# Performance work log

Hardware: AMD Instinct MI355X
Metric: run time of the kernel (lower is better)

The kernel has to match this reference:

```python
import jax, jax.numpy as jnp
import numpy as np

N = 20000        # nodes
E = 320000       # edges (avg degree 16)
F_IN = 128       # node_features
F2 = 64          # second_features (per-head out dim, LSTM hidden)
H = 8            # heads
D1 = H * F2      # 512, concat output of GATConv / LSTM input
NEG_SLOPE = 0.2  # GATConv default leaky_relu slope


def _gat_conv(x, src, dst, W, att_src, att_dst, bias):
    """PyG GATConv (concat=True, self-loops added, eval-mode dropout)."""
    n = x.shape[0]
    h = (x @ W).reshape(n, H, -1)                      # [N,H,F]
    a_s = (h * att_src).sum(-1)                        # [N,H]
    a_d = (h * att_dst).sum(-1)                        # [N,H]
    e = jax.nn.leaky_relu(a_s[src] + a_d[dst], NEG_SLOPE)   # [E',H]
    m = jax.ops.segment_max(e, dst, num_segments=n)    # [N,H]
    m = jnp.where(jnp.isfinite(m), m, 0.0)
    ex = jnp.exp(e - m[dst])
    denom = jax.ops.segment_sum(ex, dst, num_segments=n)
    alpha = ex / (denom[dst] + 1e-16)                  # [E',H]
    msg = h[src] * alpha[:, :, None]                   # [E',H,F]
    out = jax.ops.segment_sum(msg, dst, num_segments=n)  # [N,H,F]
    return out.reshape(n, -1) + bias                   # [N,H*F]


def _lstm_step(x, W_ih, W_hh, b_ih, b_hh):
    """Single-timestep PyTorch LSTM with zero initial (h0, c0). x: [N,D1]."""
    h0 = jnp.zeros((x.shape[0], F2), x.dtype)
    gates = x @ W_ih.T + b_ih + h0 @ W_hh.T + b_hh     # [N,4*F2]
    i, f, g, o = jnp.split(gates, 4, axis=-1)
    c = jax.nn.sigmoid(f) * 0.0 + jax.nn.sigmoid(i) * jnp.tanh(g)
    h = jax.nn.sigmoid(o) * jnp.tanh(c)
    return h, (h, c)


def setup_inputs() -> dict:
    key = jax.random.key(0)
    ks = jax.random.split(key, 16)

    def glorot(k, shape, fan_in):
        return jax.random.normal(k, shape, jnp.float32) * (1.0 / np.sqrt(fan_in))

    return {
        "x": jax.random.normal(ks[0], (N, F_IN), jnp.float32),
        "edge_index": jax.random.randint(ks[1], (2, E), 0, N, jnp.int32),
        "edge_weight": jax.random.uniform(ks[2], (E,), jnp.float32),
        # GATConv 1: F_IN -> H*F2
        "W1": glorot(ks[3], (F_IN, H * F2), F_IN),
        "att_src1": glorot(ks[4], (H, F2), F2),
        "att_dst1": glorot(ks[5], (H, F2), F2),
        "bias1": jnp.zeros((H * F2,), jnp.float32),
        # LSTM: input D1 -> hidden F2
        "W_ih": glorot(ks[6], (4 * F2, D1), D1),
        "W_hh": glorot(ks[7], (4 * F2, F2), F2),
        "b_ih": jnp.zeros((4 * F2,), jnp.float32),
        "b_hh": jnp.zeros((4 * F2,), jnp.float32),
        # GATConv 2: F2 -> H*F2
        "W2": glorot(ks[8], (F2, H * F2), F2),
        "att_src2": glorot(ks[9], (H, F2), F2),
        "att_dst2": glorot(ks[10], (H, F2), F2),
        "bias2": jnp.zeros((H * F2,), jnp.float32),
    }


def reference(x, edge_index, edge_weight, W1, att_src1, att_dst1, bias1,
              W_ih, W_hh, b_ih, b_hh, W2, att_src2, att_dst2, bias2):
    # edge_weight is accepted but unused, matching the original forward.
    loops = jnp.arange(N, dtype=edge_index.dtype)
    src = jnp.concatenate([edge_index[0], loops])      # add self-loops (PyG default)
    dst = jnp.concatenate([edge_index[1], loops])

    h = _gat_conv(x, src, dst, W1, att_src1, att_dst1, bias1)   # [N,512]
    h, hidden2 = _lstm_step(h, W_ih, W_hh, b_ih, b_hh)          # [N,64]
    h = jax.nn.relu(h)
    h = _gat_conv(h, src, dst, W2, att_src2, att_dst2, bias2)   # [N,512]
    return jax.nn.softmax(h, axis=1)
```

## Files before the change

kernel.cpp:

```cpp
#include <hip/hip_runtime.h>
#include <math.h>
#include <stdint.h>


__global__ void count_kernel(const int* __restrict__ dst, int* __restrict__ deg, int E) {
  int i = blockIdx.x * 256 + threadIdx.x;
  if (i < E) atomicAdd(&deg[dst[i]], 1);
}

__global__ void scan_kernel(const int* __restrict__ deg, int* __restrict__ rowptr, int n) {
  __shared__ int buf[1024];
  const int tid = threadIdx.x;
  const int i0 = tid * 20;
  int v[20];
  int tsum = 0;
#pragma unroll
  for (int k = 0; k < 20; ++k) {
    int i = i0 + k;
    v[k] = (i < n) ? (deg[i] + 1) : 0;
    tsum += v[k];
  }
  int incl = tsum;
  buf[tid] = incl;
  __syncthreads();
  for (int s = 1; s < 1024; s <<= 1) {
    int t = (tid >= (unsigned)s) ? buf[tid - s] : 0;
    __syncthreads();
    incl += t;
    buf[tid] = incl;
    __syncthreads();
  }
  int excl = incl - tsum;
#pragma unroll
  for (int k = 0; k < 20; ++k) {
    int i = i0 + k;
    if (i < n) rowptr[i] = excl;
    excl += v[k];
  }
  if (tid == 1023) rowptr[n] = incl;
}

__global__ void scatter_kernel(const int* __restrict__ src, const int* __restrict__ dst,
                               const int* __restrict__ rowptr, int* __restrict__ wp,
                               int* __restrict__ col, int E, int n) {
  int i = blockIdx.x * 256 + threadIdx.x;
  if (i < E) {
    int d = dst[i];
    int p = rowptr[d] + atomicAdd(&wp[d], 1);
    col[p] = src[i];
  } else if (i < E + n) {
    int d = i - E;
    int p = rowptr[d] + atomicAdd(&wp[d], 1);
    col[p] = d;
  }
}


__device__ __forceinline__ uint16_t bf16r(float x) {
  uint32_t u = __float_as_uint(x);
  return (uint16_t)((u + 0x7FFFu + ((u >> 16) & 1u)) >> 16);
}
__device__ __forceinline__ void bfsplit(float x, uint16_t& h, uint16_t& l) {
  h = bf16r(x);
  float hf = __uint_as_float((uint32_t)h << 16);
  l = bf16r(x - hf);
}
__device__ __forceinline__ void store4split(uint16_t* oh, uint16_t* ol, float4 v) {
  ushort4 h, l;
  bfsplit(v.x, h.x, l.x); bfsplit(v.y, h.y, l.y);
  bfsplit(v.z, h.z, l.z); bfsplit(v.w, h.w, l.w);
  *reinterpret_cast<ushort4*>(oh) = h;
  *reinterpret_cast<ushort4*>(ol) = l;
}

__device__ __forceinline__ void gload16(const uint16_t* g, uint16_t* l) {
  __builtin_amdgcn_global_load_lds(
      (const __attribute__((address_space(1))) uint32_t*)g,
      (__attribute__((address_space(3))) uint32_t*)l, 16, 0, 0);
}

using bf16x8 = __attribute__((ext_vector_type(8))) short;
using f32x4  = __attribute__((ext_vector_type(4))) float;


template <bool SPLIT_OUT>
__global__ __launch_bounds__(256) void gemm_mfma(
    const uint16_t* __restrict__ Ah, const uint16_t* __restrict__ Al,
    const uint16_t* __restrict__ Bh, const uint16_t* __restrict__ Bl,
    float* __restrict__ C, uint16_t* __restrict__ Ch, uint16_t* __restrict__ Cl,
    const float* __restrict__ bias,
    int M, int K, int lda, int aZ, int bZ, int ldc, int cZ, int biasZ) {
  constexpr int BM = 64, BN = 64, BK = 64;
  constexpr int PL = BM * BK;
  __shared__ __align__(16) uint16_t sAh[2 * PL], sAl[2 * PL];
  __shared__ __align__(16) uint16_t sBh[2 * PL], sBl[2 * PL];
  const int z = blockIdx.z;
  Ah += (size_t)z * aZ; Al += (size_t)z * aZ;
  Bh += (size_t)z * bZ; Bl += (size_t)z * bZ;
  const int tid = threadIdx.x;
  const int wid = tid >> 6, lane = tid & 63;
  int L = blockIdx.x + gridDim.x * blockIdx.y;
  int nwg = gridDim.x * gridDim.y;
  int q = nwg >> 3, r = nwg & 7;
  int xcd = L & 7, gix = L >> 3;
  int base = (xcd < r) ? xcd * (q + 1) : r * (q + 1) + (xcd - r) * q;
  int w = base + gix;
  const int bm = (w / gridDim.x) * BM;
  const int bn = (w % gridDim.x) * BN;
  const int fr = lane & 15;
  const int kg = lane >> 4;
  const int mbase = wid * 16;
  f32x4 acc[4] = {};

  auto stage = [&](int sb, int k0) {
#pragma unroll
    for (int j = 0; j < 2; ++j) {
      int idx = (wid * 2 + j) * 64 + lane;
      int row = idx >> 3, c = idx & 7;
      int rg = min(bm + row, M - 1);
      size_t goA = (size_t)rg * lda + k0 + ((c ^ (row & 7)) << 3);
      uint16_t* ldst = sAh + sb * PL + (wid * 2 + j) * 512;
      gload16(Ah + goA, ldst);
      gload16(Al + goA, sAl + sb * PL + (wid * 2 + j) * 512);
      size_t goB = (size_t)(bn + row) * K + k0 + ((c ^ (row & 7)) << 3);
      gload16(Bh + goB, sBh + sb * PL + (wid * 2 + j) * 512);
      gload16(Bl + goB, sBl + sb * PL + (wid * 2 + j) * 512);
    }
  };

  stage(0, 0);
  __syncthreads();
  int buf = 0;
  for (int k0 = 0; k0 < K; k0 += BK) {
    const bool more = (k0 + BK) < K;
    if (more) stage(buf ^ 1, k0 + BK);
    const char* pAh = (const char*)sAh + buf * (PL * 2);
    const char* pAl = (const char*)sAl + buf * (PL * 2);
    const char* pBh = (const char*)sBh + buf * (PL * 2);
    const char* pBl = (const char*)sBl + buf * (PL * 2);
#pragma unroll
    for (int ks = 0; ks < 2; ++ks) {
      const int kc = ks * 4 + kg;
      bf16x8 ah, al, bh[4], bl[4];
      {
        int m = mbase + fr;
        int off = m * 128 + ((kc ^ (m & 7)) << 4);
        ah = *reinterpret_cast<const bf16x8*>(pAh + off);
        al = *reinterpret_cast<const bf16x8*>(pAl + off);
      }
#pragma unroll
      for (int j = 0; j < 4; ++j) {
        int n = j * 16 + fr;
        int off = n * 128 + ((kc ^ (n & 7)) << 4);
        bh[j] = *reinterpret_cast<const bf16x8*>(pBh + off);
        bl[j] = *reinterpret_cast<const bf16x8*>(pBl + off);
      }
#pragma unroll
      for (int j = 0; j < 4; ++j) {
        acc[j] = __builtin_amdgcn_mfma_f32_16x16x32_bf16(ah, bh[j], acc[j], 0, 0, 0);
        acc[j] = __builtin_amdgcn_mfma_f32_16x16x32_bf16(al, bh[j], acc[j], 0, 0, 0);
        acc[j] = __builtin_amdgcn_mfma_f32_16x16x32_bf16(ah, bl[j], acc[j], 0, 0, 0);
      }
    }
    if (more) {
      __syncthreads();
      buf ^= 1;
    }
  }
  float bz[4];
#pragma unroll
  for (int j = 0; j < 4; ++j)
    bz[j] = bias ? bias[(size_t)z * biasZ + bn + j * 16 + fr] : 0.f;
  if (SPLIT_OUT) {
    Ch += (size_t)z * cZ;
    Cl += (size_t)z * cZ;
  } else {
    C += (size_t)z * cZ;
  }
  {
    int mr = bm + mbase + kg * 4;
#pragma unroll
    for (int rr = 0; rr < 4; ++rr) {
      int m = mr + rr;
      if (m < M) {
#pragma unroll
        for (int j = 0; j < 4; ++j) {
          float v = acc[j][rr] + bz[j];
          size_t o = (size_t)m * ldc + bn + j * 16 + fr;
          if (SPLIT_OUT) {
            uint16_t h, l;
            bfsplit(v, h, l);
            Ch[o] = h; Cl[o] = l;
          } else {
            C[o] = v;
          }
        }
      }
    }
  }
}


__global__ void prep_all_kernel(const float* __restrict__ W_ih, const float* __restrict__ b_ih,
                                const float* __restrict__ b_hh, const float* __restrict__ W1,
                                const float* __restrict__ as1, const float* __restrict__ ad1,
                                const float* __restrict__ W2, const float* __restrict__ as2,
                                const float* __restrict__ ad2,
                                int* __restrict__ degwp,
                                uint16_t* __restrict__ Wtbh, uint16_t* __restrict__ Wtbl,
                                uint16_t* __restrict__ Bt1h, uint16_t* __restrict__ Bt1l,
                                uint16_t* __restrict__ Bt2h, uint16_t* __restrict__ Bt2l,
                                float* __restrict__ bsum, float* __restrict__ watt1,
                                float* __restrict__ watt2, int n2) {
  int idx = blockIdx.x * 256 + threadIdx.x;
  if (idx < n2) {
    degwp[idx] = 0;
    return;
  }
  int t = idx - n2;
  if (t < 98304) {
    int jp = t >> 9, k = t & 511;
    int j = (jp < 64) ? jp : jp + 64;
    uint16_t h, l;
    bfsplit(W_ih[(size_t)j * 512 + k], h, l);
    Wtbh[t] = h; Wtbl[t] = l;
    return;
  }
  t -= 98304;
  if (t < 65536) {
    int n = t >> 7, k = t & 127;
    uint16_t h, l;
    bfsplit(W1[(size_t)k * 512 + n], h, l);
    Bt1h[t] = h; Bt1l[t] = l;
    return;
  }
  t -= 65536;
  if (t < 32768) {
    int n = t >> 6, k = t & 63;
    uint16_t h, l;
    bfsplit(W2[(size_t)k * 512 + n], h, l);
    Bt2h[t] = h; Bt2l[t] = l;
    return;
  }
  t -= 32768;
  if (t < 192) {
    int j = (t < 64) ? t : t + 64;
    bsum[t] = b_ih[j] + b_hh[j];
    return;
  }
  t -= 192;
  if (t < 2048) {
    int f = t >> 4, c = t & 15;
    int k = c & 7;
    const float* att = ((c < 8) ? as1 : ad1) + k * 64;
    const float* w = W1 + (size_t)f * 512 + k * 64;
    float s = 0.f;
#pragma unroll
    for (int j = 0; j < 64; ++j) s = fmaf(w[j], att[j], s);
    watt1[t] = s;
    return;
  }
  t -= 2048;
  if (t < 1024) {
    int f = t >> 4, c = t & 15;
    int k = c & 7;
    const float* att = ((c < 8) ? as2 : ad2) + k * 64;
    const float* w = W2 + (size_t)f * 512 + k * 64;
    float s = 0.f;
#pragma unroll
    for (int j = 0; j < 64; ++j) s = fmaf(w[j], att[j], s);
    watt2[t] = s;
  }
}


template <int F>
__global__ __launch_bounds__(256) void attcoef_kernel(
    const float* __restrict__ feat, const float* __restrict__ watt,
    float* __restrict__ a_s, float* __restrict__ a_d, int n) {
  __shared__ float rows[16 * F];
  __shared__ float wbuf[F * 16];
  const int n0 = blockIdx.x * 16;
  const int tid = threadIdx.x;
  if (n0 + 16 <= n) {
    const float4* g = reinterpret_cast<const float4*>(feat + (size_t)n0 * F);
    float4* l = reinterpret_cast<float4*>(rows);
    for (int i = tid; i < 16 * F / 4; i += 256) l[i] = g[i];
  } else {
    for (int i = tid; i < 16 * F; i += 256) {
      int r = i / F;
      rows[i] = (n0 + r < n) ? feat[(size_t)(n0 + r) * F + (i - r * F)] : 0.f;
    }
  }
  {
    const float4* g = reinterpret_cast<const float4*>(watt);
    float4* l = reinterpret_cast<float4*>(wbuf);
    for (int i = tid; i < F * 16 / 4; i += 256) l[i] = g[i];
  }
  __syncthreads();
  const int local = tid >> 4, c = tid & 15;
  float s = 0.f;
#pragma unroll 8
  for (int f = 0; f < F; ++f) s = fmaf(rows[local * F + f], wbuf[f * 16 + c], s);
  const int node = n0 + local;
  if (node < n) {
    if (c < 8) a_s[(size_t)node * 8 + c] = s;
    else       a_d[(size_t)node * 8 + (c - 8)] = s;
  }
}


template <int F>
__global__ __launch_bounds__(256) void gat_aggregate_wave(
    const float* __restrict__ feat, const float* __restrict__ a_s,
    const float* __restrict__ a_d, const int* __restrict__ rowptr,
    const int* __restrict__ col, uint16_t* __restrict__ aggH,
    uint16_t* __restrict__ aggL, int n) {
  constexpr int F4 = F / 4;
  constexpr int HPG = (F == 128) ? 4 : 2;
  __shared__ float s_alpha[4][8][8];
  __shared__ int s_cols[4][8];
  const int wid = threadIdx.x >> 6;
  const int lane = threadIdx.x & 63;
  const int node = blockIdx.x * 4 + wid;
  if (node >= n) return;
  const int start = rowptr[node];
  const int deg = rowptr[node + 1] - start;
  const int j = lane >> 3;
  const int h = lane & 7;
  const float adh = a_d[(size_t)node * 8 + h];
  float den = 0.f;
  for (int e = j; e < deg; e += 8) {
    int s = col[start + e];
    float v = a_s[(size_t)s * 8 + h] + adh;
    v = (v > 0.f) ? v : 0.2f * v;
    den += __expf(v);
  }
  den += __shfl_xor(den, 8);
  den += __shfl_xor(den, 16);
  den += __shfl_xor(den, 32);
  const float inv = 1.f / (den + 1e-16f);
  const int f4 = lane & (F4 - 1);
  const int hbase = (lane / F4) * HPG;
  float4 acc0 = make_float4(0.f, 0.f, 0.f, 0.f);
  float4 acc1 = make_float4(0.f, 0.f, 0.f, 0.f);
  float4 acc2 = make_float4(0.f, 0.f, 0.f, 0.f);
  float4 acc3 = make_float4(0.f, 0.f, 0.f, 0.f);
  for (int c0 = 0; c0 < deg; c0 += 8) {
    float aval = 0.f;
    int sj = 0;
    if (c0 + j < deg) {
      sj = col[start + c0 + j];
      float v = a_s[(size_t)sj * 8 + h] + adh;
      v = (v > 0.f) ? v : 0.2f * v;
      aval = __expf(v) * inv;
    }
    s_alpha[wid][j][h] = aval;
    if (h == 0) s_cols[wid][j] = sj;
    __builtin_amdgcn_wave_barrier();
    const int ce = min(8, deg - c0);
    for (int e = 0; e < ce; ++e) {
      int s = s_cols[wid][e];
      float4 fv = *reinterpret_cast<const float4*>(feat + (size_t)s * F + f4 * 4);
      if constexpr (HPG == 4) {
        float4 al = *reinterpret_cast<const float4*>(&s_alpha[wid][e][hbase]);
        acc0.x = fmaf(al.x, fv.x, acc0.x); acc0.y = fmaf(al.x, fv.y, acc0.y);
        acc0.z = fmaf(al.x, fv.z, acc0.z); acc0.w = fmaf(al.x, fv.w, acc0.w);
        acc1.x = fmaf(al.y, fv.x, acc1.x); acc1.y = fmaf(al.y, fv.y, acc1.y);
        acc1.z = fmaf(al.y, fv.z, acc1.z); acc1.w = fmaf(al.y, fv.w, acc1.w);
        acc2.x = fmaf(al.z, fv.x, acc2.x); acc2.y = fmaf(al.z, fv.y, acc2.y);
        acc2.z = fmaf(al.z, fv.z, acc2.z); acc2.w = fmaf(al.z, fv.w, acc2.w);
        acc3.x = fmaf(al.w, fv.x, acc3.x); acc3.y = fmaf(al.w, fv.y, acc3.y);
        acc3.z = fmaf(al.w, fv.z, acc3.z); acc3.w = fmaf(al.w, fv.w, acc3.w);
      } else {
        float2 al = *reinterpret_cast<const float2*>(&s_alpha[wid][e][hbase]);
        acc0.x = fmaf(al.x, fv.x, acc0.x); acc0.y = fmaf(al.x, fv.y, acc0.y);
        acc0.z = fmaf(al.x, fv.z, acc0.z); acc0.w = fmaf(al.x, fv.w, acc0.w);
        acc1.x = fmaf(al.y, fv.x, acc1.x); acc1.y = fmaf(al.y, fv.y, acc1.y);
        acc1.z = fmaf(al.y, fv.z, acc1.z); acc1.w = fmaf(al.y, fv.w, acc1.w);
      }
    }
    __builtin_amdgcn_wave_barrier();
  }
  size_t basep = (size_t)node * 8 * F + (size_t)hbase * F + f4 * 4;
  store4split(aggH + basep, aggL + basep, acc0);
  store4split(aggH + basep + F, aggL + basep + F, acc1);
  if constexpr (HPG == 4) {
    store4split(aggH + basep + 2 * F, aggL + basep + 2 * F, acc2);
    store4split(aggH + basep + 3 * F, aggL + basep + 3 * F, acc3);
  }
}


__global__ __launch_bounds__(256) void lstm_act_attcoef_kernel(
    const float* __restrict__ gates, const float* __restrict__ bsum,
    const float* __restrict__ watt2, float* __restrict__ h2,
    float* __restrict__ a_s2, float* __restrict__ a_d2, int n) {
  __shared__ float h2t[4][64];
  __shared__ float wbuf[64 * 16];
  const int tid = threadIdx.x;
  reinterpret_cast<float4*>(wbuf)[tid] = reinterpret_cast<const float4*>(watt2)[tid];
  const int nl = tid >> 6, j = tid & 63;
  const int node = blockIdx.x * 4 + nl;
  float hv = 0.f;
  if (node < n) {
    const float* g0 = gates + (size_t)node * 192;
    float iv = g0[j] + bsum[j];
    float gv = g0[64 + j] + bsum[64 + j];
    float ov = g0[128 + j] + bsum[128 + j];
    float c = (1.f / (1.f + __expf(-iv))) * tanhf(gv);
    hv = fmaxf((1.f / (1.f + __expf(-ov))) * tanhf(c), 0.f);
    h2[(size_t)node * 64 + j] = hv;
  }
  h2t[nl][j] = hv;
  __syncthreads();
  if (j < 16 && node < n) {
    float s = 0.f;
#pragma unroll 16
    for (int f = 0; f < 64; ++f) s = fmaf(h2t[nl][f], wbuf[f * 16 + j], s);
    if (j < 8) a_s2[(size_t)node * 8 + j] = s;
    else       a_d2[(size_t)node * 8 + (j - 8)] = s;
  }
}


__global__ __launch_bounds__(256) void softmax512_wave(const float* __restrict__ in,
                                                       float* __restrict__ out, int n) {
  const int wid = threadIdx.x >> 6, lane = threadIdx.x & 63;
  const int node = blockIdx.x * 4 + wid;
  if (node >= n) return;
  const float4* ip = reinterpret_cast<const float4*>(in + (size_t)node * 512);
  float4 v0 = ip[lane];
  float4 v1 = ip[64 + lane];
  float m = fmaxf(fmaxf(fmaxf(v0.x, v0.y), fmaxf(v0.z, v0.w)),
                  fmaxf(fmaxf(v1.x, v1.y), fmaxf(v1.z, v1.w)));
#pragma unroll
  for (int d = 1; d < 64; d <<= 1) m = fmaxf(m, __shfl_xor(m, d));
  float4 e0, e1;
  e0.x = __expf(v0.x - m); e0.y = __expf(v0.y - m);
  e0.z = __expf(v0.z - m); e0.w = __expf(v0.w - m);
  e1.x = __expf(v1.x - m); e1.y = __expf(v1.y - m);
  e1.z = __expf(v1.z - m); e1.w = __expf(v1.w - m);
  float s = e0.x + e0.y + e0.z + e0.w + e1.x + e1.y + e1.z + e1.w;
#pragma unroll
  for (int d = 1; d < 64; d <<= 1) s += __shfl_xor(s, d);
  float inv = 1.f / s;
  e0.x *= inv; e0.y *= inv; e0.z *= inv; e0.w *= inv;
  e1.x *= inv; e1.y *= inv; e1.z *= inv; e1.w *= inv;
  float4* op = reinterpret_cast<float4*>(out + (size_t)node * 512);
  op[lane] = e0;
  op[64 + lane] = e1;
}


extern "C" void kernel_launch(void* const* d_in, const int* in_sizes, int n_in,
                              void* d_out, int out_size, void* d_ws, size_t ws_size,
                              hipStream_t stream) {
  const float* x      = (const float*)d_in[0];
  const int*   ei     = (const int*)d_in[1];
  const float* W1     = (const float*)d_in[3];
  const float* att_s1 = (const float*)d_in[4];
  const float* att_d1 = (const float*)d_in[5];
  const float* bias1  = (const float*)d_in[6];
  const float* W_ih   = (const float*)d_in[7];
  const float* b_ih   = (const float*)d_in[9];
  const float* b_hh   = (const float*)d_in[10];
  const float* W2     = (const float*)d_in[11];
  const float* att_s2 = (const float*)d_in[12];
  const float* att_d2 = (const float*)d_in[13];
  const float* bias2  = (const float*)d_in[14];
  float* out = (float*)d_out;

  const int N = in_sizes[0] / 128;
  const int E = in_sizes[1] / 2;
  const int* src = ei;
  const int* dst = ei + E;

  char* p = (char*)d_ws;
  auto alloc = [&](size_t bytes) {
    char* r = p;
    p += (bytes + 255) & ~(size_t)255;
    return r;
  };
  char* slotA = alloc((size_t)N * 4096);
  char* slotB = alloc((size_t)N * 2048);
  float* a_s1 = (float*)alloc((size_t)N * 8 * 4);
  float* a_d1 = (float*)alloc((size_t)N * 8 * 4);
  float* a_s2 = (float*)alloc((size_t)N * 8 * 4);
  float* a_d2 = (float*)alloc((size_t)N * 8 * 4);
  float* watt1 = (float*)alloc(128 * 16 * 4);
  float* watt2 = (float*)alloc(64 * 16 * 4);
  uint16_t* Wtbh = (uint16_t*)alloc((size_t)192 * 512 * 2);
  uint16_t* Wtbl = (uint16_t*)alloc((size_t)192 * 512 * 2);
  uint16_t* Bt1h = (uint16_t*)alloc((size_t)512 * 128 * 2);
  uint16_t* Bt1l = (uint16_t*)alloc((size_t)512 * 128 * 2);
  uint16_t* Bt2h = (uint16_t*)alloc((size_t)512 * 64 * 2);
  uint16_t* Bt2l = (uint16_t*)alloc((size_t)512 * 64 * 2);
  float* bsum = (float*)alloc(192 * 4);
  int* deg    = (int*)alloc((size_t)2 * N * 4);
  int* wp     = deg + N;
  int* rowptr = (int*)alloc((size_t)(N + 1) * 4);
  int* col    = (int*)alloc((size_t)(E + N) * 4);

  uint16_t* agg1h = (uint16_t*)slotA;
  uint16_t* agg1l = agg1h + (size_t)N * 1024;
  float* gates2 = (float*)slotA;
  float* h2 = (float*)(slotA + (size_t)N * 768);
  uint16_t* agg2h = (uint16_t*)(slotA + (size_t)N * 1024);
  uint16_t* agg2l = agg2h + (size_t)N * 512;
  uint16_t* g1h = (uint16_t*)slotB;
  uint16_t* g1l = g1h + (size_t)N * 512;
  float* h3p = (float*)slotB;

  {
    int total = 2 * N + 98304 + 65536 + 32768 + 192 + 2048 + 1024;
    prep_all_kernel<<<(total + 255) / 256, 256, 0, stream>>>(
        W_ih, b_ih, b_hh, W1, att_s1, att_d1, W2, att_s2, att_d2,
        deg, Wtbh, Wtbl, Bt1h, Bt1l, Bt2h, Bt2l, bsum, watt1, watt2, 2 * N);
  }

  count_kernel<<<(E + 255) / 256, 256, 0, stream>>>(dst, deg, E);
  scan_kernel<<<1, 1024, 0, stream>>>(deg, rowptr, N);
  scatter_kernel<<<(E + N + 255) / 256, 256, 0, stream>>>(src, dst, rowptr, wp, col, E, N);

  const int NYB = (N + 63) / 64;

  attcoef_kernel<128><<<(N + 15) / 16, 256, 0, stream>>>(x, watt1, a_s1, a_d1, N);
  gat_aggregate_wave<128><<<(N + 3) / 4, 256, 0, stream>>>(x, a_s1, a_d1, rowptr, col,
                                                           agg1h, agg1l, N);
  {
    dim3 g(1, NYB, 8);
    gemm_mfma<true><<<g, 256, 0, stream>>>(
        agg1h, agg1l, Bt1h, Bt1l, nullptr, g1h, g1l, bias1,
        N, 128, 1024, 128, 64 * 128, 512, 64, 64);
  }

  {
    dim3 g(3, NYB, 1);
    gemm_mfma<false><<<g, 256, 0, stream>>>(
        g1h, g1l, Wtbh, Wtbl, gates2, nullptr, nullptr, nullptr,
        N, 512, 512, 0, 0, 192, 0, 0);
  }
  lstm_act_attcoef_kernel<<<(N + 3) / 4, 256, 0, stream>>>(gates2, bsum, watt2,
                                                           h2, a_s2, a_d2, N);

  gat_aggregate_wave<64><<<(N + 3) / 4, 256, 0, stream>>>(h2, a_s2, a_d2, rowptr, col,
                                                          agg2h, agg2l, N);
  {
    dim3 g(1, NYB, 8);
    gemm_mfma<false><<<g, 256, 0, stream>>>(
        agg2h, agg2l, Bt2h, Bt2l, h3p, nullptr, nullptr, bias2,
        N, 64, 512, 64, 64 * 64, 512, 64, 64);
  }
  softmax512_wave<<<(N + 3) / 4, 256, 0, stream>>>(h3p, out, N);
}
```

Before: 324.4 us.

## Fuse softmax denominator into single aggregation pass and split edges across lane groups

The GAT aggregation kernel no longer makes a separate pass over each node's edges to compute the softmax denominator. It accumulates unnormalized exp-weighted features and the denominator in one pass, then normalizes at the end. Lanes are also regrouped so each group handles different edges for all 8 heads, with cross-group shuffle reductions before the store. This removes a redundant col/a_s gather loop and reduces redundant feature loads. In exchange it uses more accumulator registers (32 floats per lane) and adds shuffle reductions at the end.

```diff
diff --git a/kernel.cpp b/kernel.cpp
--- a/kernel.cpp
+++ b/kernel.cpp
@@ -316,9 +316,10 @@
     const float* __restrict__ a_d, const int* __restrict__ rowptr,
     const int* __restrict__ col, uint16_t* __restrict__ aggH,
     uint16_t* __restrict__ aggL, int n) {
-  constexpr int F4 = F / 4;
-  constexpr int HPG = (F == 128) ? 4 : 2;
-  __shared__ float s_alpha[4][8][8];
+  constexpr int FL = F / 4;
+  constexpr int GROUPS = 64 / FL;
+  constexpr int HPW = 8 / GROUPS;
+  __shared__ float s_ex[4][8][8];
   __shared__ int s_cols[4][8];
   const int wid = threadIdx.x >> 6;
   const int lane = threadIdx.x & 63;
@@ -328,66 +329,68 @@
   const int deg = rowptr[node + 1] - start;
   const int j = lane >> 3;
   const int h = lane & 7;
+  const int grp = lane / FL;
+  const int fl = lane % FL;
   const float adh = a_d[(size_t)node * 8 + h];
-  float den = 0.f;
-  for (int e = j; e < deg; e += 8) {
-    int s = col[start + e];
-    float v = a_s[(size_t)s * 8 + h] + adh;
-    v = (v > 0.f) ? v : 0.2f * v;
-    den += __expf(v);
-  }
-  den += __shfl_xor(den, 8);
-  den += __shfl_xor(den, 16);
-  den += __shfl_xor(den, 32);
-  const float inv = 1.f / (den + 1e-16f);
-  const int f4 = lane & (F4 - 1);
-  const int hbase = (lane / F4) * HPG;
-  float4 acc0 = make_float4(0.f, 0.f, 0.f, 0.f);
-  float4 acc1 = make_float4(0.f, 0.f, 0.f, 0.f);
-  float4 acc2 = make_float4(0.f, 0.f, 0.f, 0.f);
-  float4 acc3 = make_float4(0.f, 0.f, 0.f, 0.f);
+  float dpart = 0.f;
+  float acc[8][4];
+#pragma unroll
+  for (int q = 0; q < 8; ++q)
+#pragma unroll
+    for (int t = 0; t < 4; ++t) acc[q][t] = 0.f;
+
   for (int c0 = 0; c0 < deg; c0 += 8) {
-    float aval = 0.f;
+    float ex = 0.f;
     int sj = 0;
     if (c0 + j < deg) {
       sj = col[start + c0 + j];
       float v = a_s[(size_t)sj * 8 + h] + adh;
       v = (v > 0.f) ? v : 0.2f * v;
-      aval = __expf(v) * inv;
-    }
-    s_alpha[wid][j][h] = aval;
+      ex = __expf(v);
+    }
+    s_ex[wid][j][h] = ex;
     if (h == 0) s_cols[wid][j] = sj;
+    dpart += ex;
     __builtin_amdgcn_wave_barrier();
     const int ce = min(8, deg - c0);
-    for (int e = 0; e < ce; ++e) {
+    for (int e = grp; e < ce; e += GROUPS) {
       int s = s_cols[wid][e];
-      float4 fv = *reinterpret_cast<const float4*>(feat + (size_t)s * F + f4 * 4);
-      if constexpr (HPG == 4) {
-        float4 al = *reinterpret_cast<const float4*>(&s_alpha[wid][e][hbase]);
-        acc0.x = fmaf(al.x, fv.x, acc0.x); acc0.y = fmaf(al.x, fv.y, acc0.y);
-        acc0.z = fmaf(al.x, fv.z, acc0.z); acc0.w = fmaf(al.x, fv.w, acc0.w);
-        acc1.x = fmaf(al.y, fv.x, acc1.x); acc1.y = fmaf(al.y, fv.y, acc1.y);
-        acc1.z = fmaf(al.y, fv.z, acc1.z); acc1.w = fmaf(al.y, fv.w, acc1.w);
-        acc2.x = fmaf(al.z, fv.x, acc2.x); acc2.y = fmaf(al.z, fv.y, acc2.y);
-        acc2.z = fmaf(al.z, fv.z, acc2.z); acc2.w = fmaf(al.z, fv.w, acc2.w);
-        acc3.x = fmaf(al.w, fv.x, acc3.x); acc3.y = fmaf(al.w, fv.y, acc3.y);
-        acc3.z = fmaf(al.w, fv.z, acc3.z); acc3.w = fmaf(al.w, fv.w, acc3.w);
-      } else {
-        float2 al = *reinterpret_cast<const float2*>(&s_alpha[wid][e][hbase]);
-        acc0.x = fmaf(al.x, fv.x, acc0.x); acc0.y = fmaf(al.x, fv.y, acc0.y);
-        acc0.z = fmaf(al.x, fv.z, acc0.z); acc0.w = fmaf(al.x, fv.w, acc0.w);
-        acc1.x = fmaf(al.y, fv.x, acc1.x); acc1.y = fmaf(al.y, fv.y, acc1.y);
-        acc1.z = fmaf(al.y, fv.z, acc1.z); acc1.w = fmaf(al.y, fv.w, acc1.w);
+      float4 fv = *reinterpret_cast<const float4*>(feat + (size_t)s * F + fl * 4);
+      float al[8];
+      *reinterpret_cast<float4*>(&al[0]) = *reinterpret_cast<const float4*>(&s_ex[wid][e][0]);
+      *reinterpret_cast<float4*>(&al[4]) = *reinterpret_cast<const float4*>(&s_ex[wid][e][4]);
+#pragma unroll
+      for (int q = 0; q < 8; ++q) {
+        acc[q][0] = fmaf(al[q], fv.x, acc[q][0]);
+        acc[q][1] = fmaf(al[q], fv.y, acc[q][1]);
+        acc[q][2] = fmaf(al[q], fv.z, acc[q][2]);
+        acc[q][3] = fmaf(al[q], fv.w, acc[q][3]);
       }
     }
     __builtin_amdgcn_wave_barrier();
   }
-  size_t basep = (size_t)node * 8 * F + (size_t)hbase * F + f4 * 4;
-  store4split(aggH + basep, aggL + basep, acc0);
-  store4split(aggH + basep + F, aggL + basep + F, acc1);
-  if constexpr (HPG == 4) {
-    store4split(aggH + basep + 2 * F, aggL + basep + 2 * F, acc2);
-    store4split(aggH + basep + 3 * F, aggL + basep + 3 * F, acc3);
+  dpart += __shfl_xor(dpart, 8);
+  dpart += __shfl_xor(dpart, 16);
+  dpart += __shfl_xor(dpart, 32);
+#pragma unroll
+  for (int q = 0; q < 8; ++q)
+#pragma unroll
+    for (int t = 0; t < 4; ++t) {
+      float v = acc[q][t];
+      if (GROUPS == 4) v += __shfl_xor(v, 16);
+      v += __shfl_xor(v, 32);
+      acc[q][t] = v;
+    }
+#pragma unroll
+  for (int q = 0; q < 8; ++q) {
+    float dq = __shfl(dpart, q);
+    if (q / HPW == grp) {
+      float dinv = 1.f / (dq + 1e-16f);
+      size_t off = (size_t)node * 8 * F + (size_t)q * F + fl * 4;
+      float4 o = make_float4(acc[q][0] * dinv, acc[q][1] * dinv,
+                             acc[q][2] * dinv, acc[q][3] * dinv);
+      store4split(aggH + off, aggL + off, o);
+    }
   }
 }
 
```

After: 327.2 us. Within noise of the previous version (+0.9%).
